# Optimization experiments

Hardware: AMD Instinct MI355X
Metric: run time of the kernel (lower is better)

The kernel has to match this reference:

```python
import jax, jax.numpy as jnp
import numpy as np

B_SZ, L, DIM, H_DIM, D_STATE, K = 2, 2048, 768, 1536, 16, 4


def setup_inputs() -> dict:
    key = jax.random.key(0)
    ks = jax.random.split(key, 16)
    sc = 0.02
    inp = {
        "x": jax.random.normal(ks[0], (B_SZ, L, DIM), dtype=jnp.float32),
        "W1": jax.random.normal(ks[1], (DIM, H_DIM), dtype=jnp.float32) * sc,
        "b1": jnp.zeros((H_DIM,), dtype=jnp.float32),
        "W2": jax.random.normal(ks[2], (DIM, H_DIM), dtype=jnp.float32) * sc,
        "b2": jnp.zeros((H_DIM,), dtype=jnp.float32),
        "conv_w": jax.random.normal(ks[3], (H_DIM, 1, K), dtype=jnp.float32) * sc,  # depthwise, OIH
        "conv_b": jnp.zeros((H_DIM,), dtype=jnp.float32),
        "Wf": jax.random.normal(ks[4], (H_DIM, DIM), dtype=jnp.float32) * sc,
        "bf": jnp.zeros((DIM,), dtype=jnp.float32),
        "A": jnp.tile(jnp.arange(1, D_STATE + 1, dtype=jnp.float32), (H_DIM, 1)),  # [d, s]
        "WB": jax.random.normal(ks[5], (H_DIM, D_STATE), dtype=jnp.float32) * sc,
        "bB": jnp.zeros((D_STATE,), dtype=jnp.float32),
        "WC": jax.random.normal(ks[6], (H_DIM, D_STATE), dtype=jnp.float32) * sc,
        "bC": jnp.zeros((D_STATE,), dtype=jnp.float32),
        "WD": jax.random.normal(ks[7], (H_DIM, H_DIM), dtype=jnp.float32) * sc,
        "bD": jnp.zeros((H_DIM,), dtype=jnp.float32),
        "Dvec": jnp.ones((H_DIM,), dtype=jnp.float32),
    }
    return inp


def _forward(x, W1, b1, W2, b2, conv_w, conv_b, Wf, bf, A, WB, bB, WC, bC, WD, bD, Dvec):
    b, l, _ = x.shape
    k = conv_w.shape[-1]
    a = x @ W1 + b1                      # [b, l, d]
    g = jax.nn.silu(x @ W2 + b2)         # [b, l, d]  (silu(linear_2(x)))
    # depthwise causal conv1d: torch pads both sides by k-1 then slices [:l]
    xc = jnp.swapaxes(a, 1, 2)           # [b, d, l]
    ac = jax.lax.conv_general_dilated(
        xc, conv_w, window_strides=(1,), padding=[(k - 1, 0)],
        feature_group_count=xc.shape[1],
        dimension_numbers=("NCH", "OIH", "NCH"),
    ) + conv_b[None, :, None]
    a = jax.nn.silu(jnp.swapaxes(ac, 1, 2))          # [b, l, d]
    delta = jax.nn.softplus(Dvec + a @ WD + bD)       # [b, l, d]
    Bm = a @ WB + bB                                  # [b, l, s]
    # discretized dynamics
    A_ = jnp.exp(-A)[None, None] * delta[..., None]   # [b, l, d, s]
    X_ = Bm[:, :, None, :] * delta[..., None] * a[..., None]  # [b, l, d, s]
    # sequential selective scan: h_t = A_t * h_{t-1} + X_t
    A_t = jnp.moveaxis(A_, 1, 0)                      # [l, b, d, s]
    X_t = jnp.moveaxis(X_, 1, 0)
    def step(h, AX):
        At, Xt = AX
        h = At * h + Xt
        return h, h
    h0 = jnp.zeros(A_t.shape[1:], dtype=x.dtype)
    _, hs = jax.lax.scan(step, h0, (A_t, X_t))
    hid = jnp.moveaxis(hs, 0, 1)                      # [b, l, d, s]
    # NOTE: original computes einsum(hid, C) + D*a then overwrites it; the
    # returned output is linear_f(a * silu(linear_2(x))).
    output = (a * g) @ Wf + bf                        # [b, l, dim]
    return output, hid, a[..., 1:]


def reference(x, W1, b1, W2, b2, conv_w, conv_b, Wf, bf, A, WB, bB, WC, bC, WD, bD, Dvec):
    return _forward(x, W1, b1, W2, b2, conv_w, conv_b, Wf, bf, A, WB, bB, WC, bC, WD, bD, Dvec)
```

## Files before the change

### kernel.cpp

```cpp
#include <hip/hip_runtime.h>
#include <hip/hip_bf16.h>
#include <cstddef>

constexpr int B_SZ  = 2;
constexpr int LSEQ  = 2048;
constexpr int DIM   = 768;
constexpr int H_DIM = 1536;
constexpr int DST   = 16;
constexpr int KW    = 4;
constexpr int MROWS = B_SZ * LSEQ;
constexpr int HS    = H_DIM * DST;

constexpr int CCH  = 16;
constexpr int CLEN = LSEQ / CCH;

using short8 = __attribute__((ext_vector_type(8))) short;
using f32x4  = __attribute__((ext_vector_type(4))) float;

__device__ __forceinline__ short f2bf(float v) {
    union { float f; unsigned u; } x; x.f = v;
    unsigned r = (x.u + 0x7FFFu + ((x.u >> 16) & 1u)) >> 16;
    return (short)r;
}
__device__ __forceinline__ float bf2f(short s) {
    union { unsigned u; float f; } x; x.u = ((unsigned)(unsigned short)s) << 16;
    return x.f;
}

__global__ __launch_bounds__(256) void wsplit_k(
    const float* __restrict__ W, unsigned short* __restrict__ Wh,
    unsigned short* __restrict__ Wl, int K, int N)
{
    __shared__ float t[32][33];
    const int k0 = blockIdx.x * 32, n0 = blockIdx.y * 32;
    const int r = threadIdx.x >> 5, c = threadIdx.x & 31;
#pragma unroll
    for (int p = 0; p < 4; ++p)
        t[r + p * 8][c] = W[(size_t)(k0 + r + p * 8) * N + n0 + c];
    __syncthreads();
#pragma unroll
    for (int p = 0; p < 4; ++p) {
        int rr = r + p * 8;
        float v = t[c][rr];
        short hi = f2bf(v);
        short lo = f2bf(v - bf2f(hi));
        size_t o = (size_t)(n0 + rr) * K + k0 + c;
        Wh[o] = (unsigned short)hi;
        Wl[o] = (unsigned short)lo;
    }
}

template <int EPI, bool AMUL>
__global__ __launch_bounds__(256) void gemm_mx(
    const float* __restrict__ A, const float* __restrict__ A2,
    const unsigned short* __restrict__ WBh, const unsigned short* __restrict__ WBl,
    const float* __restrict__ bias, const float* __restrict__ extra,
    float* __restrict__ C, int M, int N, int K)
{
    constexpr int SK = 40;
    __shared__ short Ah[128 * SK], Al[128 * SK];
    __shared__ short Bh[128 * SK], Bl[128 * SK];

    const int tid  = threadIdx.x;
    const int n0   = blockIdx.x * 128, m0 = blockIdx.y * 128;
    const int wave = tid >> 6, lane = tid & 63;
    const int wm   = wave >> 1, wn = wave & 1;
    const int lr   = lane & 15, kg = lane >> 4;

    const int srow = tid >> 1;
    const int skh  = (tid & 1) * 16;

    f32x4 acc[4][4] = {};

    for (int k0 = 0; k0 < K; k0 += 32) {
        {
            const float* ap = A + (size_t)(m0 + srow) * K + k0 + skh;
            float va[16];
            *reinterpret_cast<float4*>(&va[0])  = *reinterpret_cast<const float4*>(ap + 0);
            *reinterpret_cast<float4*>(&va[4])  = *reinterpret_cast<const float4*>(ap + 4);
            *reinterpret_cast<float4*>(&va[8])  = *reinterpret_cast<const float4*>(ap + 8);
            *reinterpret_cast<float4*>(&va[12]) = *reinterpret_cast<const float4*>(ap + 12);
            if (AMUL) {
                const float* gp = A2 + (size_t)(m0 + srow) * K + k0 + skh;
                float vg[16];
                *reinterpret_cast<float4*>(&vg[0])  = *reinterpret_cast<const float4*>(gp + 0);
                *reinterpret_cast<float4*>(&vg[4])  = *reinterpret_cast<const float4*>(gp + 4);
                *reinterpret_cast<float4*>(&vg[8])  = *reinterpret_cast<const float4*>(gp + 8);
                *reinterpret_cast<float4*>(&vg[12]) = *reinterpret_cast<const float4*>(gp + 12);
#pragma unroll
                for (int i = 0; i < 16; ++i) va[i] *= vg[i];
            }
            short sh[16], sl[16];
#pragma unroll
            for (int i = 0; i < 16; ++i) {
                sh[i] = f2bf(va[i]);
                sl[i] = f2bf(va[i] - bf2f(sh[i]));
            }
            int ab = srow * SK + skh;
            *reinterpret_cast<short8*>(&Ah[ab + 0]) = *reinterpret_cast<short8*>(&sh[0]);
            *reinterpret_cast<short8*>(&Ah[ab + 8]) = *reinterpret_cast<short8*>(&sh[8]);
            *reinterpret_cast<short8*>(&Al[ab + 0]) = *reinterpret_cast<short8*>(&sl[0]);
            *reinterpret_cast<short8*>(&Al[ab + 8]) = *reinterpret_cast<short8*>(&sl[8]);
        }
        {
            size_t bo = (size_t)(n0 + srow) * K + k0 + skh;
            int bb = srow * SK + skh;
            *reinterpret_cast<short8*>(&Bh[bb + 0]) = *reinterpret_cast<const short8*>(WBh + bo);
            *reinterpret_cast<short8*>(&Bh[bb + 8]) = *reinterpret_cast<const short8*>(WBh + bo + 8);
            *reinterpret_cast<short8*>(&Bl[bb + 0]) = *reinterpret_cast<const short8*>(WBl + bo);
            *reinterpret_cast<short8*>(&Bl[bb + 8]) = *reinterpret_cast<const short8*>(WBl + bo + 8);
        }
        __syncthreads();

        short8 fa_h[4], fa_l[4], fb_h[4], fb_l[4];
#pragma unroll
        for (int f = 0; f < 4; ++f) {
            int aoff = (wm * 64 + f * 16 + lr) * SK + kg * 8;
            int boff = (wn * 64 + f * 16 + lr) * SK + kg * 8;
            fa_h[f] = *reinterpret_cast<const short8*>(&Ah[aoff]);
            fa_l[f] = *reinterpret_cast<const short8*>(&Al[aoff]);
            fb_h[f] = *reinterpret_cast<const short8*>(&Bh[boff]);
            fb_l[f] = *reinterpret_cast<const short8*>(&Bl[boff]);
        }
#pragma unroll
        for (int mf = 0; mf < 4; ++mf)
#pragma unroll
            for (int nf = 0; nf < 4; ++nf)
                acc[mf][nf] = __builtin_amdgcn_mfma_f32_16x16x32_bf16(
                    fa_h[mf], fb_h[nf], acc[mf][nf], 0, 0, 0);
#pragma unroll
        for (int mf = 0; mf < 4; ++mf)
#pragma unroll
            for (int nf = 0; nf < 4; ++nf)
                acc[mf][nf] = __builtin_amdgcn_mfma_f32_16x16x32_bf16(
                    fa_h[mf], fb_l[nf], acc[mf][nf], 0, 0, 0);
#pragma unroll
        for (int mf = 0; mf < 4; ++mf)
#pragma unroll
            for (int nf = 0; nf < 4; ++nf)
                acc[mf][nf] = __builtin_amdgcn_mfma_f32_16x16x32_bf16(
                    fa_l[mf], fb_h[nf], acc[mf][nf], 0, 0, 0);
        __syncthreads();
    }

    float bv[4], ev[4];
#pragma unroll
    for (int nf = 0; nf < 4; ++nf) {
        int col = n0 + wn * 64 + nf * 16 + lr;
        bv[nf] = bias[col];
        ev[nf] = (EPI == 2) ? extra[col] : 0.f;
    }
#pragma unroll
    for (int mf = 0; mf < 4; ++mf)
#pragma unroll
        for (int nf = 0; nf < 4; ++nf) {
            int col = n0 + wn * 64 + nf * 16 + lr;
#pragma unroll
            for (int r = 0; r < 4; ++r) {
                int mrow = m0 + wm * 64 + mf * 16 + kg * 4 + r;
                float v = acc[mf][nf][r] + bv[nf];
                if (EPI == 1) v = v / (1.f + expf(-v));
                if (EPI == 2) {
                    float t2 = ev[nf] + v;
                    v = fmaxf(t2, 0.f) + log1pf(expf(-fabsf(t2)));
                }
                C[(size_t)mrow * N + col] = v;
            }
        }
}

__global__ __launch_bounds__(256) void conv_k(
    const float* __restrict__ apre, const float* __restrict__ cw,
    const float* __restrict__ cb, float* __restrict__ aout,
    float* __restrict__ trim)
{
    int idx = blockIdx.x * 256 + threadIdx.x;
    int d  = idx % H_DIM;
    int bt = idx / H_DIM;
    int t  = bt % LSEQ;

    float4 w = *reinterpret_cast<const float4*>(cw + (size_t)d * KW);
    float acc = cb[d];
    if (t >= KW - 1) {
        const float* base = apre + (size_t)(bt - 3) * H_DIM + d;
        acc += base[0] * w.x;
        acc += base[H_DIM] * w.y;
        acc += base[2 * H_DIM] * w.z;
        acc += base[3 * H_DIM] * w.w;
    } else {
        const float* wp = reinterpret_cast<const float*>(&w);
#pragma unroll
        for (int j = 0; j < KW; ++j) {
            int tt = t + j - (KW - 1);
            if (tt >= 0) acc += apre[(size_t)(bt + j - 3) * H_DIM + d] * wp[j];
        }
    }
    float sv = acc / (1.f + expf(-acc));
    aout[idx] = sv;
    if (d >= 1)
        __builtin_nontemporal_store(sv, &trim[(size_t)bt * (H_DIM - 1) + d - 1]);
}

__global__ __launch_bounds__(256) void bm_k(
    const float* __restrict__ a, const float* __restrict__ WB,
    const float* __restrict__ bB, float* __restrict__ Bm)
{
    int g = blockIdx.x * 256 + threadIdx.x;
    int row = g >> 4, n = g & 15;
    const float* ar = a + (size_t)row * H_DIM;
    float a0 = 0.f, a1 = 0.f, a2 = 0.f, a3 = 0.f;
    for (int k = 0; k < H_DIM; k += 4) {
        a0 = fmaf(ar[k],     WB[(size_t)(k)*DST + n],     a0);
        a1 = fmaf(ar[k + 1], WB[(size_t)(k + 1)*DST + n], a1);
        a2 = fmaf(ar[k + 2], WB[(size_t)(k + 2)*DST + n], a2);
        a3 = fmaf(ar[k + 3], WB[(size_t)(k + 3)*DST + n], a3);
    }
    Bm[g] = bB[n] + ((a0 + a1) + (a2 + a3));
}

__global__ __launch_bounds__(256) void scan_a(
    const float* __restrict__ delta, const float* __restrict__ a,
    const float* __restrict__ Bm, const float* __restrict__ A,
    float* __restrict__ hend, float* __restrict__ Pout)
{
    int gtid = blockIdx.x * 256 + threadIdx.x;
    int ds = gtid % HS;
    int bc = gtid / HS;
    int c = bc % CCH, b = bc / CCH;
    int d = ds >> 4, s = ds & 15;

    float eA = expf(-A[ds]);
    float h = 0.f, P = 1.f;
    int bt0 = b * LSEQ + c * CLEN;
#pragma unroll 4
    for (int i = 0; i < CLEN; ++i) {
        int bt = bt0 + i;
        size_t ix = (size_t)bt * H_DIM + d;
        float dl = delta[ix];
        float av = a[ix];
        float bm = Bm[(size_t)bt * DST + s];
        float at = eA * dl;
        h = fmaf(at, h, bm * dl * av);
        P *= at;
    }
    size_t o = ((size_t)b * CCH + c) * HS + ds;
    hend[o] = h;
    Pout[o] = P;
}

__global__ __launch_bounds__(256) void scan_b(
    const float* __restrict__ hend, const float* __restrict__ P,
    float* __restrict__ Hinit)
{
    int gtid = blockIdx.x * 256 + threadIdx.x;
    int ds = gtid % HS;
    int b  = gtid / HS;
    float Hc = 0.f;
    for (int c = 0; c < CCH; ++c) {
        size_t o = ((size_t)b * CCH + c) * HS + ds;
        Hinit[o] = Hc;
        Hc = hend[o] + P[o] * Hc;
    }
}

__global__ __launch_bounds__(256) void scan_c(
    const float* __restrict__ delta, const float* __restrict__ a,
    const float* __restrict__ Bm, const float* __restrict__ A,
    const float* __restrict__ Hinit, float* __restrict__ hid)
{
    int gtid = blockIdx.x * 256 + threadIdx.x;
    int ds = gtid % HS;
    int bc = gtid / HS;
    int c = bc % CCH, b = bc / CCH;
    int d = ds >> 4, s = ds & 15;

    float eA = expf(-A[ds]);
    float h = Hinit[((size_t)b * CCH + c) * HS + ds];
    int bt0 = b * LSEQ + c * CLEN;
#pragma unroll 4
    for (int i = 0; i < CLEN; ++i) {
        int bt = bt0 + i;
        size_t ix = (size_t)bt * H_DIM + d;
        float dl = delta[ix];
        float av = a[ix];
        float bm = Bm[(size_t)bt * DST + s];
        float at = eA * dl;
        h = fmaf(at, h, bm * dl * av);
        __builtin_nontemporal_store(h, &hid[(size_t)bt * HS + ds]);
    }
}

extern "C" void kernel_launch(void* const* d_in, const int* in_sizes, int n_in,
                              void* d_out, int out_size, void* d_ws, size_t ws_size,
                              hipStream_t stream)
{
    const float* x      = (const float*)d_in[0];
    const float* W1     = (const float*)d_in[1];
    const float* b1     = (const float*)d_in[2];
    const float* W2     = (const float*)d_in[3];
    const float* b2     = (const float*)d_in[4];
    const float* conv_w = (const float*)d_in[5];
    const float* conv_b = (const float*)d_in[6];
    const float* Wf     = (const float*)d_in[7];
    const float* bf     = (const float*)d_in[8];
    const float* A      = (const float*)d_in[9];
    const float* WB     = (const float*)d_in[10];
    const float* bB     = (const float*)d_in[11];
    const float* WD     = (const float*)d_in[14];
    const float* bD     = (const float*)d_in[15];
    const float* Dvec   = (const float*)d_in[16];

    float* out = (float*)d_out;
    constexpr size_t OUT_HID  = (size_t)MROWS * DIM;
    constexpr size_t OUT_TRIM = OUT_HID + (size_t)MROWS * HS;
    float* out_y    = out;
    float* out_hid  = out + OUT_HID;
    float* out_trim = out + OUT_TRIM;

    constexpr size_t MH = (size_t)MROWS * H_DIM;
    float* a_pre = out_hid;
    float* g     = out_hid + MH;
    unsigned short* wsp = (unsigned short*)(out_hid + 2 * MH);
    constexpr size_t WSMALL = (size_t)H_DIM * DIM;
    constexpr size_t WBIG   = (size_t)H_DIM * H_DIM;
    unsigned short* W1h = wsp;
    unsigned short* W1l = W1h + WSMALL;
    unsigned short* W2h = W1l + WSMALL;
    unsigned short* W2l = W2h + WSMALL;
    unsigned short* WDh = W2l + WSMALL;
    unsigned short* WDl = WDh + WBIG;
    unsigned short* Wfh = WDl + WBIG;
    unsigned short* Wfl = Wfh + WSMALL;

    float* ws      = (float*)d_ws;
    float* a_ws    = ws;
    float* delta   = a_ws  + MH;
    float* Bm      = delta + MH;
    float* hend    = Bm    + (size_t)MROWS * DST;
    float* Pprod   = hend  + (size_t)B_SZ * HS * CCH;
    float* Hinit   = Pprod + (size_t)B_SZ * HS * CCH;

    dim3 blk(256);

    wsplit_k<<<dim3(DIM / 32, H_DIM / 32), blk, 0, stream>>>(W1, W1h, W1l, DIM, H_DIM);
    wsplit_k<<<dim3(DIM / 32, H_DIM / 32), blk, 0, stream>>>(W2, W2h, W2l, DIM, H_DIM);
    wsplit_k<<<dim3(H_DIM / 32, H_DIM / 32), blk, 0, stream>>>(WD, WDh, WDl, H_DIM, H_DIM);
    wsplit_k<<<dim3(H_DIM / 32, DIM / 32), blk, 0, stream>>>(Wf, Wfh, Wfl, H_DIM, DIM);

    gemm_mx<0, false><<<dim3(H_DIM / 128, MROWS / 128), blk, 0, stream>>>(
        x, nullptr, W1h, W1l, b1, nullptr, a_pre, MROWS, H_DIM, DIM);
    gemm_mx<1, false><<<dim3(H_DIM / 128, MROWS / 128), blk, 0, stream>>>(
        x, nullptr, W2h, W2l, b2, nullptr, g, MROWS, H_DIM, DIM);
    conv_k<<<(MROWS * H_DIM) / 256, blk, 0, stream>>>(a_pre, conv_w, conv_b, a_ws, out_trim);
    gemm_mx<2, false><<<dim3(H_DIM / 128, MROWS / 128), blk, 0, stream>>>(
        a_ws, nullptr, WDh, WDl, bD, Dvec, delta, MROWS, H_DIM, H_DIM);
    bm_k<<<(MROWS * DST) / 256, blk, 0, stream>>>(a_ws, WB, bB, Bm);
    gemm_mx<0, true><<<dim3(DIM / 128, MROWS / 128), blk, 0, stream>>>(
        a_ws, g, Wfh, Wfl, bf, nullptr, out_y, MROWS, DIM, H_DIM);
    scan_a<<<(B_SZ * CCH * HS) / 256, blk, 0, stream>>>(delta, a_ws, Bm, A, hend, Pprod);
    scan_b<<<(B_SZ * HS) / 256, blk, 0, stream>>>(hend, Pprod, Hinit);
    scan_c<<<(B_SZ * CCH * HS) / 256, blk, 0, stream>>>(delta, a_ws, Bm, A, Hinit, out_hid);
}
```

Measured before the change: 941.0 us.

## Pre-split GEMM activations into bf16 hi/lo buffers and retile to 128x64 blocks

Activation matrices are now split into bf16 high/low halves once, before the GEMMs run: x in a new kernel, and a and a*g inside the conv kernel. Previously every GEMM block redid the fp32-to-bf16 conversion on each tile it loaded. The GEMM becomes a 128-thread kernel with a 128x64 tile, where each wave covers 64 rows and all 64 columns. This removes redundant conversion work and the separate AMUL multiply, and launches more blocks. In exchange it writes and rereads extra bf16 buffers, which adds global memory traffic, and it halves the waves per block.

```diff
diff --git a/kernel.cpp b/kernel.cpp
--- a/kernel.cpp
+++ b/kernel.cpp
@@ -50,73 +50,74 @@
     }
 }
 
-template <int EPI, bool AMUL>
-__global__ __launch_bounds__(256) void gemm_mx(
-    const float* __restrict__ A, const float* __restrict__ A2,
-    const unsigned short* __restrict__ WBh, const unsigned short* __restrict__ WBl,
+__global__ __launch_bounds__(256) void xsplit_k(
+    const float* __restrict__ X, unsigned short* __restrict__ Xh,
+    unsigned short* __restrict__ Xl, size_t n8)
+{
+    size_t g = (size_t)blockIdx.x * 256 + threadIdx.x;
+    if (g >= n8) return;
+    const float* xp = X + g * 8;
+    float v[8];
+    *reinterpret_cast<float4*>(&v[0]) = *reinterpret_cast<const float4*>(xp);
+    *reinterpret_cast<float4*>(&v[4]) = *reinterpret_cast<const float4*>(xp + 4);
+    short h[8], l[8];
+#pragma unroll
+    for (int i = 0; i < 8; ++i) {
+        h[i] = f2bf(v[i]);
+        l[i] = f2bf(v[i] - bf2f(h[i]));
+    }
+    *reinterpret_cast<short8*>(Xh + g * 8) = *reinterpret_cast<short8*>(&h[0]);
+    *reinterpret_cast<short8*>(Xl + g * 8) = *reinterpret_cast<short8*>(&l[0]);
+}
+
+template <int EPI>
+__global__ __launch_bounds__(128) void gemm_bf(
+    const unsigned short* __restrict__ Ahp, const unsigned short* __restrict__ Alp,
+    const unsigned short* __restrict__ Bhp, const unsigned short* __restrict__ Blp,
     const float* __restrict__ bias, const float* __restrict__ extra,
     float* __restrict__ C, int M, int N, int K)
 {
     constexpr int SK = 40;
     __shared__ short Ah[128 * SK], Al[128 * SK];
-    __shared__ short Bh[128 * SK], Bl[128 * SK];
+    __shared__ short Bh[64 * SK],  Bl[64 * SK];
 
     const int tid  = threadIdx.x;
-    const int n0   = blockIdx.x * 128, m0 = blockIdx.y * 128;
+    const int n0   = blockIdx.x * 64, m0 = blockIdx.y * 128;
     const int wave = tid >> 6, lane = tid & 63;
-    const int wm   = wave >> 1, wn = wave & 1;
     const int lr   = lane & 15, kg = lane >> 4;
-
-    const int srow = tid >> 1;
-    const int skh  = (tid & 1) * 16;
 
     f32x4 acc[4][4] = {};
 
     for (int k0 = 0; k0 < K; k0 += 32) {
         {
-            const float* ap = A + (size_t)(m0 + srow) * K + k0 + skh;
-            float va[16];
-            *reinterpret_cast<float4*>(&va[0])  = *reinterpret_cast<const float4*>(ap + 0);
-            *reinterpret_cast<float4*>(&va[4])  = *reinterpret_cast<const float4*>(ap + 4);
-            *reinterpret_cast<float4*>(&va[8])  = *reinterpret_cast<const float4*>(ap + 8);
-            *reinterpret_cast<float4*>(&va[12]) = *reinterpret_cast<const float4*>(ap + 12);
-            if (AMUL) {
-                const float* gp = A2 + (size_t)(m0 + srow) * K + k0 + skh;
-                float vg[16];
-                *reinterpret_cast<float4*>(&vg[0])  = *reinterpret_cast<const float4*>(gp + 0);
-                *reinterpret_cast<float4*>(&vg[4])  = *reinterpret_cast<const float4*>(gp + 4);
-                *reinterpret_cast<float4*>(&vg[8])  = *reinterpret_cast<const float4*>(gp + 8);
-                *reinterpret_cast<float4*>(&vg[12]) = *reinterpret_cast<const float4*>(gp + 12);
-#pragma unroll
-                for (int i = 0; i < 16; ++i) va[i] *= vg[i];
+            const unsigned short* ah = Ahp + (size_t)(m0 + tid) * K + k0;
+            const unsigned short* al = Alp + (size_t)(m0 + tid) * K + k0;
+            int ab = tid * SK;
+#pragma unroll
+            for (int i = 0; i < 4; ++i) {
+                *reinterpret_cast<short8*>(&Ah[ab + 8 * i]) =
+                    *reinterpret_cast<const short8*>(ah + 8 * i);
+                *reinterpret_cast<short8*>(&Al[ab + 8 * i]) =
+                    *reinterpret_cast<const short8*>(al + 8 * i);
             }
-            short sh[16], sl[16];
-#pragma unroll
-            for (int i = 0; i < 16; ++i) {
-                sh[i] = f2bf(va[i]);
-                sl[i] = f2bf(va[i] - bf2f(sh[i]));
-            }
-            int ab = srow * SK + skh;
-            *reinterpret_cast<short8*>(&Ah[ab + 0]) = *reinterpret_cast<short8*>(&sh[0]);
-            *reinterpret_cast<short8*>(&Ah[ab + 8]) = *reinterpret_cast<short8*>(&sh[8]);
-            *reinterpret_cast<short8*>(&Al[ab + 0]) = *reinterpret_cast<short8*>(&sl[0]);
-            *reinterpret_cast<short8*>(&Al[ab + 8]) = *reinterpret_cast<short8*>(&sl[8]);
         }
         {
-            size_t bo = (size_t)(n0 + srow) * K + k0 + skh;
-            int bb = srow * SK + skh;
-            *reinterpret_cast<short8*>(&Bh[bb + 0]) = *reinterpret_cast<const short8*>(WBh + bo);
-            *reinterpret_cast<short8*>(&Bh[bb + 8]) = *reinterpret_cast<const short8*>(WBh + bo + 8);
-            *reinterpret_cast<short8*>(&Bl[bb + 0]) = *reinterpret_cast<const short8*>(WBl + bo);
-            *reinterpret_cast<short8*>(&Bl[bb + 8]) = *reinterpret_cast<const short8*>(WBl + bo + 8);
+            int brow = tid & 63;
+            const unsigned short* bp =
+                (tid < 64 ? Bhp : Blp) + (size_t)(n0 + brow) * K + k0;
+            short* bd = (tid < 64 ? Bh : Bl) + brow * SK;
+#pragma unroll
+            for (int i = 0; i < 4; ++i)
+                *reinterpret_cast<short8*>(&bd[8 * i]) =
+                    *reinterpret_cast<const short8*>(bp + 8 * i);
         }
         __syncthreads();
 
         short8 fa_h[4], fa_l[4], fb_h[4], fb_l[4];
 #pragma unroll
         for (int f = 0; f < 4; ++f) {
-            int aoff = (wm * 64 + f * 16 + lr) * SK + kg * 8;
-            int boff = (wn * 64 + f * 16 + lr) * SK + kg * 8;
+            int aoff = (wave * 64 + f * 16 + lr) * SK + kg * 8;
+            int boff = (f * 16 + lr) * SK + kg * 8;
             fa_h[f] = *reinterpret_cast<const short8*>(&Ah[aoff]);
             fa_l[f] = *reinterpret_cast<const short8*>(&Al[aoff]);
             fb_h[f] = *reinterpret_cast<const short8*>(&Bh[boff]);
@@ -146,7 +147,7 @@
     float bv[4], ev[4];
 #pragma unroll
     for (int nf = 0; nf < 4; ++nf) {
-        int col = n0 + wn * 64 + nf * 16 + lr;
+        int col = n0 + nf * 16 + lr;
         bv[nf] = bias[col];
         ev[nf] = (EPI == 2) ? extra[col] : 0.f;
     }
@@ -154,10 +155,10 @@
     for (int mf = 0; mf < 4; ++mf)
 #pragma unroll
         for (int nf = 0; nf < 4; ++nf) {
-            int col = n0 + wn * 64 + nf * 16 + lr;
+            int col = n0 + nf * 16 + lr;
 #pragma unroll
             for (int r = 0; r < 4; ++r) {
-                int mrow = m0 + wm * 64 + mf * 16 + kg * 4 + r;
+                int mrow = m0 + wave * 64 + mf * 16 + kg * 4 + r;
                 float v = acc[mf][nf][r] + bv[nf];
                 if (EPI == 1) v = v / (1.f + expf(-v));
                 if (EPI == 2) {
@@ -171,7 +172,10 @@
 
 __global__ __launch_bounds__(256) void conv_k(
     const float* __restrict__ apre, const float* __restrict__ cw,
-    const float* __restrict__ cb, float* __restrict__ aout,
+    const float* __restrict__ cb, const float* __restrict__ g,
+    float* __restrict__ aout,
+    unsigned short* __restrict__ ah, unsigned short* __restrict__ al,
+    unsigned short* __restrict__ ph, unsigned short* __restrict__ pl,
     float* __restrict__ trim)
 {
     int idx = blockIdx.x * 256 + threadIdx.x;
@@ -197,6 +201,13 @@
     }
     float sv = acc / (1.f + expf(-acc));
     aout[idx] = sv;
+    short h = f2bf(sv);
+    ah[idx] = (unsigned short)h;
+    al[idx] = (unsigned short)f2bf(sv - bf2f(h));
+    float pv = sv * g[idx];
+    short hp = f2bf(pv);
+    ph[idx] = (unsigned short)hp;
+    pl[idx] = (unsigned short)f2bf(pv - bf2f(hp));
     if (d >= 1)
         __builtin_nontemporal_store(sv, &trim[(size_t)bt * (H_DIM - 1) + d - 1]);
 }
@@ -318,19 +329,19 @@
     float* out_trim = out + OUT_TRIM;
 
     constexpr size_t MH = (size_t)MROWS * H_DIM;
+    constexpr size_t MD = (size_t)MROWS * DIM;
     float* a_pre = out_hid;
     float* g     = out_hid + MH;
     unsigned short* wsp = (unsigned short*)(out_hid + 2 * MH);
     constexpr size_t WSMALL = (size_t)H_DIM * DIM;
     constexpr size_t WBIG   = (size_t)H_DIM * H_DIM;
-    unsigned short* W1h = wsp;
-    unsigned short* W1l = W1h + WSMALL;
-    unsigned short* W2h = W1l + WSMALL;
-    unsigned short* W2l = W2h + WSMALL;
-    unsigned short* WDh = W2l + WSMALL;
-    unsigned short* WDl = WDh + WBIG;
-    unsigned short* Wfh = WDl + WBIG;
-    unsigned short* Wfl = Wfh + WSMALL;
+    unsigned short* W1h = wsp;            unsigned short* W1l = W1h + WSMALL;
+    unsigned short* W2h = W1l + WSMALL;   unsigned short* W2l = W2h + WSMALL;
+    unsigned short* WDh = W2l + WSMALL;   unsigned short* WDl = WDh + WBIG;
+    unsigned short* Wfh = WDl + WBIG;     unsigned short* Wfl = Wfh + WSMALL;
+    unsigned short* xh  = Wfl + WSMALL;   unsigned short* xl  = xh + MD;
+    unsigned short* ah  = xl + MD;        unsigned short* al  = ah + MH;
+    unsigned short* ph  = al + MH;        unsigned short* pl  = ph + MH;
 
     float* ws      = (float*)d_ws;
     float* a_ws    = ws;
@@ -341,22 +352,25 @@
     float* Hinit   = Pprod + (size_t)B_SZ * HS * CCH;
 
     dim3 blk(256);
+    dim3 gblk(128);
 
     wsplit_k<<<dim3(DIM / 32, H_DIM / 32), blk, 0, stream>>>(W1, W1h, W1l, DIM, H_DIM);
     wsplit_k<<<dim3(DIM / 32, H_DIM / 32), blk, 0, stream>>>(W2, W2h, W2l, DIM, H_DIM);
     wsplit_k<<<dim3(H_DIM / 32, H_DIM / 32), blk, 0, stream>>>(WD, WDh, WDl, H_DIM, H_DIM);
     wsplit_k<<<dim3(H_DIM / 32, DIM / 32), blk, 0, stream>>>(Wf, Wfh, Wfl, H_DIM, DIM);
-
-    gemm_mx<0, false><<<dim3(H_DIM / 128, MROWS / 128), blk, 0, stream>>>(
-        x, nullptr, W1h, W1l, b1, nullptr, a_pre, MROWS, H_DIM, DIM);
-    gemm_mx<1, false><<<dim3(H_DIM / 128, MROWS / 128), blk, 0, stream>>>(
-        x, nullptr, W2h, W2l, b2, nullptr, g, MROWS, H_DIM, DIM);
-    conv_k<<<(MROWS * H_DIM) / 256, blk, 0, stream>>>(a_pre, conv_w, conv_b, a_ws, out_trim);
-    gemm_mx<2, false><<<dim3(H_DIM / 128, MROWS / 128), blk, 0, stream>>>(
-        a_ws, nullptr, WDh, WDl, bD, Dvec, delta, MROWS, H_DIM, H_DIM);
+    xsplit_k<<<(unsigned)((MD / 8 + 255) / 256), blk, 0, stream>>>(x, xh, xl, MD / 8);
+
+    gemm_bf<0><<<dim3(H_DIM / 64, MROWS / 128), gblk, 0, stream>>>(
+        xh, xl, W1h, W1l, b1, nullptr, a_pre, MROWS, H_DIM, DIM);
+    gemm_bf<1><<<dim3(H_DIM / 64, MROWS / 128), gblk, 0, stream>>>(
+        xh, xl, W2h, W2l, b2, nullptr, g, MROWS, H_DIM, DIM);
+    conv_k<<<(MROWS * H_DIM) / 256, blk, 0, stream>>>(
+        a_pre, conv_w, conv_b, g, a_ws, ah, al, ph, pl, out_trim);
+    gemm_bf<2><<<dim3(H_DIM / 64, MROWS / 128), gblk, 0, stream>>>(
+        ah, al, WDh, WDl, bD, Dvec, delta, MROWS, H_DIM, H_DIM);
     bm_k<<<(MROWS * DST) / 256, blk, 0, stream>>>(a_ws, WB, bB, Bm);
-    gemm_mx<0, true><<<dim3(DIM / 128, MROWS / 128), blk, 0, stream>>>(
-        a_ws, g, Wfh, Wfl, bf, nullptr, out_y, MROWS, DIM, H_DIM);
+    gemm_bf<0><<<dim3(DIM / 64, MROWS / 128), gblk, 0, stream>>>(
+        ph, pl, Wfh, Wfl, bf, nullptr, out_y, MROWS, DIM, H_DIM);
     scan_a<<<(B_SZ * CCH * HS) / 256, blk, 0, stream>>>(delta, a_ws, Bm, A, hend, Pprod);
     scan_b<<<(B_SZ * HS) / 256, blk, 0, stream>>>(hend, Pprod, Hinit);
     scan_c<<<(B_SZ * CCH * HS) / 256, blk, 0, stream>>>(delta, a_ws, Bm, A, Hinit, out_hid);
```

Result: slower. 1.022 ms (+8.6%).
